# Kernel optimization log

Measured on AMD Instinct MI355X. Metric: run time of the kernel, lower is better.

## Reference

```python
import jax, jax.numpy as jnp
import numpy as np

IN_CH = 512
OUT_CH = 512
NUM_GROUPS = 32
EPS = 1e-5


def setup_inputs() -> dict:
    key = jax.random.key(0)
    ks = jax.random.split(key, 8)
    N, C, H, W = 4, IN_CH, 64, 64
    s = 0.02
    return {
        "x": jax.random.normal(ks[0], (N, C, H, W), jnp.float32),
        "gn_scale": jnp.ones((C,), jnp.float32),
        "gn_bias": jnp.zeros((C,), jnp.float32),
        "wq": jax.random.normal(ks[1], (OUT_CH, C), jnp.float32) * s,
        "bq": jnp.zeros((OUT_CH,), jnp.float32),
        "wk": jax.random.normal(ks[2], (OUT_CH, C), jnp.float32) * s,
        "bk": jnp.zeros((OUT_CH,), jnp.float32),
        "wv": jax.random.normal(ks[3], (OUT_CH, C), jnp.float32) * s,
        "bv": jnp.zeros((OUT_CH,), jnp.float32),
        "wo": jax.random.normal(ks[4], (OUT_CH, OUT_CH), jnp.float32) * s,
        "bo": jnp.zeros((OUT_CH,), jnp.float32),
    }


def _group_norm(x, scale, bias):
    # x: [N, C, H, W] -> normalize per (group, spatial)
    N, C, H, W = x.shape
    g = x.reshape(N, NUM_GROUPS, C // NUM_GROUPS, H, W)
    mean = jnp.mean(g, axis=(2, 3, 4), keepdims=True)
    var = jnp.var(g, axis=(2, 3, 4), keepdims=True)
    g = (g - mean) * jax.lax.rsqrt(var + EPS)
    h = g.reshape(N, C, H, W)
    return h * scale[None, :, None, None] + bias[None, :, None, None]


def _conv1x1(x, w, b):
    # x: [N, C_in, H, W], w: [C_out, C_in] -> [N, C_out, H, W]
    return jnp.einsum('nchw,dc->ndhw', x, w) + b[None, :, None, None]


def reference(x, gn_scale, gn_bias, wq, bq, wk, bk, wv, bv, wo, bo):
    N, C, H, W = x.shape
    L = H * W
    h = _group_norm(x, gn_scale, gn_bias)
    q = _conv1x1(h, wq, bq).reshape(N, OUT_CH, L)
    k = _conv1x1(h, wk, bk).reshape(N, OUT_CH, L)
    v = _conv1x1(h, wv, bv).reshape(N, OUT_CH, L)
    scores = jnp.einsum('nci,ncj->nij', q, k) * (OUT_CH ** -0.5)  # [N, L, L]
    att = jax.nn.softmax(scores, axis=-1)
    out = jnp.einsum('nij,ncj->nci', att, v).reshape(N, OUT_CH, H, W)
    out = _conv1x1(out, wo, bo)
    return out + x  # skip_proj is Identity since in_ch == out_ch
```

## Files before the change

### kernel.cpp

```cpp
#include <hip/hip_runtime.h>
#include <math.h>

#define NB   4
#define CCH  512
#define LL   4096
#define GRP  32
#define CPG  16
#define CL   (CCH*LL)
#define EPSV 1e-5f

typedef __bf16 bf16x8 __attribute__((ext_vector_type(8)));
typedef float  f32x4  __attribute__((ext_vector_type(4)));

#define GLOAD_LDS16(g, l) __builtin_amdgcn_global_load_lds( \
    (const __attribute__((address_space(1))) void*)(g),     \
    (__attribute__((address_space(3))) void*)(l), 16, 0, 0)

__device__ __forceinline__ int swz_slot(int row, int q) {
    return (4 * row + (q ^ (row & 3))) ^ (((row >> 2) & 1) << 2);
}
__device__ __forceinline__ void swz_src(int l, int& jj, int& cc) {
    jj = ((l >> 3) << 1) | (((l >> 2) ^ (l >> 4)) & 1);
    cc = (l & 3) ^ (jj & 3);
}

#define DPPF(x, ctrl) __builtin_bit_cast(float, \
    __builtin_amdgcn_update_dpp(0, __builtin_bit_cast(int, (x)), (ctrl), 0xf, 0xf, false))
__device__ __forceinline__ float red_max16(float x) {
    x = fmaxf(x, DPPF(x, 0xB1)); x = fmaxf(x, DPPF(x, 0x4E));
    x = fmaxf(x, DPPF(x, 0x124)); x = fmaxf(x, DPPF(x, 0x128));
    return x;
}
__device__ __forceinline__ float red_sum16(float x) {
    x += DPPF(x, 0xB1); x += DPPF(x, 0x4E);
    x += DPPF(x, 0x124); x += DPPF(x, 0x128);
    return x;
}

__global__ __launch_bounds__(1024) void gn_stats(const float* __restrict__ x,
                                                 float* __restrict__ stats) {
    int n = blockIdx.x >> 5, g = blockIdx.x & 31;
    size_t base = ((size_t)n * CCH + (size_t)g * CPG) * LL;
    const float4* xp = (const float4*)(x + base);
    const int NV = CPG * LL / 4;
    int tid = threadIdx.x;
    float s1 = 0.f, s2 = 0.f;
    for (int i = tid; i < NV; i += 1024) {
        float4 v = xp[i];
        s1 += v.x + v.y + v.z + v.w;
        s2 += v.x*v.x + v.y*v.y + v.z*v.z + v.w*v.w;
    }
    __shared__ float red[32];
    for (int o = 32; o; o >>= 1) { s1 += __shfl_down(s1, o); s2 += __shfl_down(s2, o); }
    int lane = tid & 63, w = tid >> 6;
    if (!lane) { red[w] = s1; red[16 + w] = s2; }
    __syncthreads();
    if (tid == 0) {
        float a = 0.f, b = 0.f;
        for (int i = 0; i < 16; ++i) { a += red[i]; b += red[16 + i]; }
        const float inv_n = 1.f / (float)(CPG * LL);
        float mean = a * inv_n;
        float var  = b * inv_n - mean * mean;
        stats[blockIdx.x * 2]     = mean;
        stats[blockIdx.x * 2 + 1] = rsqrtf(var + EPSV);
    }
}

__global__ __launch_bounds__(256) void gn_norm_t(const float* __restrict__ x,
    const float* __restrict__ gamma, const float* __restrict__ beta,
    const float* __restrict__ stats, __bf16* __restrict__ Ht) {
    __shared__ float T[64][65];
    int n = blockIdx.z, c0 = blockIdx.y * 64, l0 = blockIdx.x * 64;
    int tid = threadIdx.x;
    int lx = tid & 63, py = tid >> 6;
    const float* xb = x + (size_t)n * CL;
#pragma unroll
    for (int p = 0; p < 16; ++p) {
        int cl = p * 4 + py;
        int c = c0 + cl;
        int g = c >> 4;
        float mean = stats[(n * GRP + g) * 2];
        float rstd = stats[(n * GRP + g) * 2 + 1];
        float sc = gamma[c] * rstd, bi = beta[c] - mean * sc;
        float v = xb[(size_t)c * LL + l0 + lx];
        T[lx][cl] = v * sc + bi;
    }
    __syncthreads();
    __bf16* hb = Ht + (size_t)n * CL;
#pragma unroll
    for (int p = 0; p < 16; ++p) {
        int ll = p * 4 + py;
        hb[(size_t)(l0 + ll) * CCH + c0 + lx] = (__bf16)T[ll][lx];
    }
}

__global__ __launch_bounds__(256) void tobf16(const float* __restrict__ src,
                                              __bf16* __restrict__ dst, int n) {
    int i = (blockIdx.x * 256 + threadIdx.x) * 4;
    if (i < n) {
        float4 v = *(const float4*)(src + i);
        dst[i]   = (__bf16)v.x; dst[i+1] = (__bf16)v.y;
        dst[i+2] = (__bf16)v.z; dst[i+3] = (__bf16)v.w;
    }
}

#define BM 128
#define BN 128
#define BK 32

template<int EPI>
__global__ __launch_bounds__(256) void gemm_nt(
    const __bf16* __restrict__ A, const __bf16* __restrict__ B,
    void* __restrict__ Cv, int M, int N, int K,
    long bsA, long bsB, long bsC, long bsR,
    const float* __restrict__ bias, const float* __restrict__ resid, float alpha)
{
    __shared__ __align__(16) __bf16 As[BM * BK];
    __shared__ __align__(16) __bf16 Bs[BN * BK];
    const int tid = threadIdx.x;
    const int l = tid & 63, w = tid >> 6;
    const int wm = w >> 1, wn = w & 1;
    const int m0 = blockIdx.y * BM, n0 = blockIdx.x * BN;
    A += (long)blockIdx.z * bsA;
    B += (long)blockIdx.z * bsB;

    f32x4 acc[4][4];
#pragma unroll
    for (int i = 0; i < 4; ++i)
#pragma unroll
        for (int j = 0; j < 4; ++j) acc[i][j] = f32x4{0.f, 0.f, 0.f, 0.f};

    int jj, cc; swz_src(l, jj, cc);
    const int slot = swz_slot(l & 15, l >> 4);

    const __bf16* Ag = A + (size_t)(m0 + w * 16 + jj) * K + cc * 8;
    const __bf16* Bg = B + (size_t)(n0 + w * 16 + jj) * K + cc * 8;
    char* AsB = (char*)As + w * 1024;
    char* BsB = (char*)Bs + w * 1024;

    for (int k0 = 0; k0 < K; k0 += BK) {
        GLOAD_LDS16(Ag + k0,                 AsB);
        GLOAD_LDS16(Ag + k0 + (size_t)64*K,  AsB + 4096);
        GLOAD_LDS16(Bg + k0,                 BsB);
        GLOAD_LDS16(Bg + k0 + (size_t)64*K,  BsB + 4096);
        __syncthreads();
        bf16x8 ar[4], br[4];
#pragma unroll
        for (int t = 0; t < 4; ++t) {
            ar[t] = *(const bf16x8*)(As + (wm*64 + t*16) * BK + slot * 8);
            br[t] = *(const bf16x8*)(Bs + (wn*64 + t*16) * BK + slot * 8);
        }
#pragma unroll
        for (int ti = 0; ti < 4; ++ti)
#pragma unroll
            for (int tj = 0; tj < 4; ++tj)
                acc[ti][tj] = __builtin_amdgcn_mfma_f32_16x16x32_bf16(
                    ar[ti], br[tj], acc[ti][tj], 0, 0, 0);
        __syncthreads();
    }

    const long cb = (long)blockIdx.z * bsC;
#pragma unroll
    for (int ti = 0; ti < 4; ++ti) {
#pragma unroll
        for (int r = 0; r < 4; ++r) {
            int m = m0 + wm*64 + ti*16 + (l >> 4)*4 + r;
            float bv = (EPI == 2 || EPI == 4) ? bias[m] : 0.f;
#pragma unroll
            for (int tj = 0; tj < 4; ++tj) {
                int n = n0 + wn*64 + tj*16 + (l & 15);
                float v = acc[ti][tj][r];
                if (EPI == 1) v += bias[n];
                if (EPI == 2 || EPI == 4) v += bv;
                if (EPI == 4) {
                    float rs = resid[(long)blockIdx.z * bsR + (size_t)m * N + n];
                    ((float*)Cv)[cb + (size_t)m * N + n] = v + rs;
                } else {
                    ((__bf16*)Cv)[cb + (size_t)m * N + n] = (__bf16)v;
                }
            }
        }
    }
}

#define PSTR 88

__global__ __launch_bounds__(512, 2) void flash_attn(
    const __bf16* __restrict__ Qt, const __bf16* __restrict__ Kt,
    const __bf16* __restrict__ Vb, __bf16* __restrict__ Ot)
{
    __shared__ __align__(16) __bf16 Ks[16 * 64 * 32];
    __shared__ __align__(16) __bf16 Vs[2 * 512 * 32];
    __shared__ __align__(16) float  Sm[64 * 68];
    __shared__ __align__(16) __bf16 Ps[64 * PSTR];
    __shared__ float scl[64];
    __shared__ float lnv[64];

    const int tid = threadIdx.x;
    const int l = tid & 63, w = tid >> 6;
    const int wi = w & 3, kh = w >> 2;
    const int g = l >> 4, c = l & 15;
    const int b = blockIdx.x >> 6;
    const int i0 = (blockIdx.x & 63) * 64;
    const size_t bb = (size_t)b * CL;
    const float alpha = 0.044194173824159216f;

    int jj, cc; swz_src(l, jj, cc);
    const int slot = swz_slot(c, g);

    bf16x8 Qf[8];
    {
        const __bf16* Qg = Qt + bb + (size_t)(i0 + wi*16 + c) * CCH + kh*256 + g*8;
#pragma unroll
        for (int kc = 0; kc < 8; ++kc) Qf[kc] = *(const bf16x8*)(Qg + kc * 32);
    }

    f32x4 Oacc[4][4];
#pragma unroll
    for (int mi = 0; mi < 4; ++mi)
#pragma unroll
        for (int ni = 0; ni < 4; ++ni) Oacc[mi][ni] = f32x4{0.f, 0.f, 0.f, 0.f};
    float m_r[4], l_r[4];
#pragma unroll
    for (int r = 0; r < 4; ++r) { m_r[r] = -1e30f; l_r[r] = 0.f; }

    const __bf16* Kb = Kt + bb;
    const __bf16* Vg = Vb + bb;

    auto stageK = [&](int j0) {
#pragma unroll
        for (int q = 0; q < 2; ++q) {
            int kc = q * 8 + w;
#pragma unroll
            for (int p = 0; p < 4; ++p) {
                const __bf16* src = Kb + (size_t)(j0 + p*16 + jj) * CCH + kc*32 + cc*8;
                GLOAD_LDS16(src, (char*)Ks + kc*4096 + p*1024);
            }
        }
    };
    auto stageV = [&](int j0) {
#pragma unroll
        for (int jc = 0; jc < 2; ++jc)
#pragma unroll
            for (int p = 0; p < 4; ++p) {
                const __bf16* src = Vg + (size_t)(w*64 + p*16 + jj) * LL + j0 + jc*32 + cc*8;
                GLOAD_LDS16(src, (char*)Vs + jc*32768 + (w*64 + p*16)*64);
            }
    };

    stageK(0);
    for (int t = 0; t < 64; ++t) {
        __syncthreads();
        stageV(t * 64);

        f32x4 S[4];
#pragma unroll
        for (int tj = 0; tj < 4; ++tj) S[tj] = f32x4{0.f, 0.f, 0.f, 0.f};
#pragma unroll
        for (int kc = 0; kc < 8; ++kc) {
#pragma unroll
            for (int tj = 0; tj < 4; ++tj) {
                bf16x8 kf = *(const bf16x8*)(Ks + (kh*8 + kc)*2048 + tj*512 + slot*8);
                S[tj] = __builtin_amdgcn_mfma_f32_16x16x32_bf16(Qf[kc], kf, S[tj], 0, 0, 0);
            }
        }

        if (kh) {
#pragma unroll
            for (int tj = 0; tj < 4; ++tj)
#pragma unroll
                for (int r = 0; r < 4; ++r)
                    Sm[(wi*16 + g*4 + r)*68 + tj*16 + c] = S[tj][r];
        }
        __syncthreads();

        if (!kh) {
#pragma unroll
            for (int r = 0; r < 4; ++r) {
                float mt = -1e30f;
#pragma unroll
                for (int tj = 0; tj < 4; ++tj) {
                    S[tj][r] = (S[tj][r] + Sm[(wi*16 + g*4 + r)*68 + tj*16 + c]) * alpha;
                    mt = fmaxf(mt, S[tj][r]);
                }
                mt = red_max16(mt);
                float mn = fmaxf(m_r[r], mt);
                float a = __expf(m_r[r] - mn);
                m_r[r] = mn;
                int row = wi*16 + g*4 + r;
                float rs = 0.f;
#pragma unroll
                for (int tj = 0; tj < 4; ++tj) {
                    float p = __expf(S[tj][r] - mn);
                    rs += p;
                    Ps[row * PSTR + tj*16 + c] = (__bf16)p;
                }
                rs = red_sum16(rs);
                l_r[r] = l_r[r] * a + rs;
                if (c == 0) scl[row] = a;
            }
        } else {
            if (t < 63) stageK((t + 1) * 64);
        }
        __syncthreads();
        if (t < 63 && !kh) stageK((t + 1) * 64);

#pragma unroll
        for (int mi = 0; mi < 4; ++mi)
#pragma unroll
            for (int r = 0; r < 4; ++r) {
                float s = scl[mi*16 + g*4 + r];
#pragma unroll
                for (int ni = 0; ni < 4; ++ni) Oacc[mi][ni][r] *= s;
            }

#pragma unroll
        for (int jc = 0; jc < 2; ++jc) {
            bf16x8 pa[4];
#pragma unroll
            for (int mi = 0; mi < 4; ++mi)
                pa[mi] = *(const bf16x8*)(Ps + (mi*16 + c) * PSTR + jc*32 + g*8);
#pragma unroll
            for (int ni = 0; ni < 4; ++ni) {
                bf16x8 vf = *(const bf16x8*)(Vs + jc*16384 + (w*64 + ni*16)*32 + slot*8);
#pragma unroll
                for (int mi = 0; mi < 4; ++mi)
                    Oacc[mi][ni] = __builtin_amdgcn_mfma_f32_16x16x32_bf16(pa[mi], vf, Oacc[mi][ni], 0, 0, 0);
            }
        }
    }

    if (!kh && c == 0) {
#pragma unroll
        for (int r = 0; r < 4; ++r) lnv[wi*16 + g*4 + r] = 1.f / l_r[r];
    }
    __syncthreads();
#pragma unroll
    for (int mi = 0; mi < 4; ++mi) {
#pragma unroll
        for (int r = 0; r < 4; ++r) {
            int row = mi*16 + g*4 + r;
            float inv = lnv[row];
#pragma unroll
            for (int ni = 0; ni < 4; ++ni) {
                int col = w*64 + ni*16 + c;
                Ot[bb + (size_t)(i0 + row) * CCH + col] = (__bf16)(Oacc[mi][ni][r] * inv);
            }
        }
    }
}

extern "C" void kernel_launch(void* const* d_in, const int* in_sizes, int n_in,
                              void* d_out, int out_size, void* d_ws, size_t ws_size,
                              hipStream_t stream) {
    const float* x   = (const float*)d_in[0];
    const float* gnw = (const float*)d_in[1];
    const float* gnb = (const float*)d_in[2];
    const float* wq  = (const float*)d_in[3];
    const float* bq  = (const float*)d_in[4];
    const float* wk  = (const float*)d_in[5];
    const float* bk  = (const float*)d_in[6];
    const float* wv  = (const float*)d_in[7];
    const float* bv  = (const float*)d_in[8];
    const float* wo  = (const float*)d_in[9];
    const float* bo  = (const float*)d_in[10];
    float* out = (float*)d_out;

    __bf16* wsb = (__bf16*)d_ws;
    const size_t NCL = (size_t)NB * CL;
    __bf16* Ht = wsb;
    __bf16* Qt = Ht + NCL;
    __bf16* Kt = Qt + NCL;
    __bf16* Vb = Kt + NCL;
    __bf16* Ot = Vb + NCL;
    __bf16* Wb = Ot + NCL;
    float* stats = (float*)(Wb + (size_t)4 * CCH * CCH);
    __bf16* wqb = Wb;
    __bf16* wkb = Wb + (size_t)CCH * CCH;
    __bf16* wvb = Wb + (size_t)2 * CCH * CCH;
    __bf16* wob = Wb + (size_t)3 * CCH * CCH;

    tobf16<<<256, 256, 0, stream>>>(wq, wqb, CCH * CCH);
    tobf16<<<256, 256, 0, stream>>>(wk, wkb, CCH * CCH);
    tobf16<<<256, 256, 0, stream>>>(wv, wvb, CCH * CCH);
    tobf16<<<256, 256, 0, stream>>>(wo, wob, CCH * CCH);

    gn_stats<<<NB * GRP, 1024, 0, stream>>>(x, stats);
    gn_norm_t<<<dim3(LL / 64, CCH / 64, NB), 256, 0, stream>>>(x, gnw, gnb, stats, Ht);

    gemm_nt<1><<<dim3(CCH / 128, LL / 128, NB), 256, 0, stream>>>(
        Ht, wqb, Qt, LL, CCH, CCH, CL, 0, CL, 0, bq, nullptr, 1.f);
    gemm_nt<1><<<dim3(CCH / 128, LL / 128, NB), 256, 0, stream>>>(
        Ht, wkb, Kt, LL, CCH, CCH, CL, 0, CL, 0, bk, nullptr, 1.f);
    gemm_nt<2><<<dim3(LL / 128, CCH / 128, NB), 256, 0, stream>>>(
        wvb, Ht, Vb, CCH, LL, CCH, 0, CL, CL, 0, bv, nullptr, 1.f);

    flash_attn<<<dim3(NB * (LL / 64)), 512, 0, stream>>>(Qt, Kt, Vb, Ot);

    gemm_nt<4><<<dim3(LL / 128, CCH / 128, NB), 256, 0, stream>>>(
        wob, Ot, (void*)out, CCH, LL, CCH, 0, CL, CL, CL, bo, x, 1.f);
}
```

Before: 427.2 us.

## Shrink flash attention tiles to 32 queries and 32 keys with 4 waves

Restructures the flash attention kernel from 64x64 tiles with 8 waves to 32x32 tiles with 4 waves (256 threads), doubling the grid to 512 blocks with an interleaved batch/query-tile mapping. Each wave now accumulates 128 output channels, the LDS swizzle pattern is simplified, and the K prefetch is done only by the kh waves after the softmax barrier. The Oacc rescale is skipped when every row's scale factor is 1. Smaller tiles lower LDS use and may raise occupancy, but they halve reuse per loaded K/V tile and double the number of loop iterations and barriers.

```diff
diff --git a/kernel.cpp b/kernel.cpp
--- a/kernel.cpp
+++ b/kernel.cpp
@@ -17,11 +17,11 @@
     (__attribute__((address_space(3))) void*)(l), 16, 0, 0)
 
 __device__ __forceinline__ int swz_slot(int row, int q) {
-    return (4 * row + (q ^ (row & 3))) ^ (((row >> 2) & 1) << 2);
+    return 4 * row + (q ^ ((row >> 1) & 3));
 }
 __device__ __forceinline__ void swz_src(int l, int& jj, int& cc) {
-    jj = ((l >> 3) << 1) | (((l >> 2) ^ (l >> 4)) & 1);
-    cc = (l & 3) ^ (jj & 3);
+    jj = l >> 2;
+    cc = (l & 3) ^ ((l >> 3) & 3);
 }
 
 #define DPPF(x, ctrl) __builtin_bit_cast(float, \
@@ -183,25 +183,26 @@
     }
 }
 
-#define PSTR 88
-
-__global__ __launch_bounds__(512, 2) void flash_attn(
+#define PST2 40
+
+__global__ __launch_bounds__(256, 2) void flash_attn(
     const __bf16* __restrict__ Qt, const __bf16* __restrict__ Kt,
     const __bf16* __restrict__ Vb, __bf16* __restrict__ Ot)
 {
-    __shared__ __align__(16) __bf16 Ks[16 * 64 * 32];
-    __shared__ __align__(16) __bf16 Vs[2 * 512 * 32];
-    __shared__ __align__(16) float  Sm[64 * 68];
-    __shared__ __align__(16) __bf16 Ps[64 * PSTR];
-    __shared__ float scl[64];
-    __shared__ float lnv[64];
+    __shared__ __align__(16) __bf16 Ks[16 * 1024];
+    __shared__ __align__(16) __bf16 Vs[512 * 32];
+    __shared__ float  Sm[32 * 33];
+    __shared__ __align__(16) __bf16 Ps[32 * PST2];
+    __shared__ float scl[32];
+    __shared__ float lnv[32];
 
     const int tid = threadIdx.x;
     const int l = tid & 63, w = tid >> 6;
-    const int wi = w & 3, kh = w >> 2;
+    const int wi = w & 1, kh = w >> 1;
     const int g = l >> 4, c = l & 15;
-    const int b = blockIdx.x >> 6;
-    const int i0 = (blockIdx.x & 63) * 64;
+    const int b = (blockIdx.x & 7) >> 1;
+    const int qt = ((blockIdx.x >> 3) << 1) | (blockIdx.x & 1);
+    const int i0 = qt * 32;
     const size_t bb = (size_t)b * CL;
     const float alpha = 0.044194173824159216f;
 
@@ -215,11 +216,11 @@
         for (int kc = 0; kc < 8; ++kc) Qf[kc] = *(const bf16x8*)(Qg + kc * 32);
     }
 
-    f32x4 Oacc[4][4];
-#pragma unroll
-    for (int mi = 0; mi < 4; ++mi)
-#pragma unroll
-        for (int ni = 0; ni < 4; ++ni) Oacc[mi][ni] = f32x4{0.f, 0.f, 0.f, 0.f};
+    f32x4 Oacc[2][8];
+#pragma unroll
+    for (int mi = 0; mi < 2; ++mi)
+#pragma unroll
+        for (int ni = 0; ni < 8; ++ni) Oacc[mi][ni] = f32x4{0.f, 0.f, 0.f, 0.f};
     float m_r[4], l_r[4];
 #pragma unroll
     for (int r = 0; r < 4; ++r) { m_r[r] = -1e30f; l_r[r] = 0.f; }
@@ -227,106 +228,118 @@
     const __bf16* Kb = Kt + bb;
     const __bf16* Vg = Vb + bb;
 
-    auto stageK = [&](int j0) {
-#pragma unroll
-        for (int q = 0; q < 2; ++q) {
-            int kc = q * 8 + w;
-#pragma unroll
-            for (int p = 0; p < 4; ++p) {
-                const __bf16* src = Kb + (size_t)(j0 + p*16 + jj) * CCH + kc*32 + cc*8;
-                GLOAD_LDS16(src, (char*)Ks + kc*4096 + p*1024);
-            }
-        }
-    };
-    auto stageV = [&](int j0) {
-#pragma unroll
-        for (int jc = 0; jc < 2; ++jc)
-#pragma unroll
-            for (int p = 0; p < 4; ++p) {
-                const __bf16* src = Vg + (size_t)(w*64 + p*16 + jj) * LL + j0 + jc*32 + cc*8;
-                GLOAD_LDS16(src, (char*)Vs + jc*32768 + (w*64 + p*16)*64);
-            }
-    };
-
-    stageK(0);
-    for (int t = 0; t < 64; ++t) {
+    {
+        const int j0 = 0;
+#pragma unroll
+        for (int q = 0; q < 4; ++q) {
+            int kc = q * 4 + w;
+#pragma unroll
+            for (int sub = 0; sub < 2; ++sub) {
+                const __bf16* src = Kb + (size_t)(j0 + sub*16 + jj) * CCH + kc*32 + cc*8;
+                GLOAD_LDS16(src, (char*)Ks + kc*2048 + sub*1024);
+            }
+        }
+    }
+
+    for (int t = 0; t < 128; ++t) {
         __syncthreads();
-        stageV(t * 64);
-
-        f32x4 S[4];
-#pragma unroll
-        for (int tj = 0; tj < 4; ++tj) S[tj] = f32x4{0.f, 0.f, 0.f, 0.f};
+        {
+            const int j0 = t * 32;
+#pragma unroll
+            for (int p = 0; p < 8; ++p) {
+                const __bf16* src = Vg + (size_t)(w*128 + p*16 + jj) * LL + j0 + cc*8;
+                GLOAD_LDS16(src, (char*)Vs + (w*128 + p*16) * 64);
+            }
+        }
+
+        f32x4 S[2];
+        S[0] = f32x4{0.f,0.f,0.f,0.f}; S[1] = f32x4{0.f,0.f,0.f,0.f};
 #pragma unroll
         for (int kc = 0; kc < 8; ++kc) {
 #pragma unroll
-            for (int tj = 0; tj < 4; ++tj) {
-                bf16x8 kf = *(const bf16x8*)(Ks + (kh*8 + kc)*2048 + tj*512 + slot*8);
+            for (int tj = 0; tj < 2; ++tj) {
+                bf16x8 kf = *(const bf16x8*)(Ks + (kh*8 + kc)*1024 + tj*512 + slot*8);
                 S[tj] = __builtin_amdgcn_mfma_f32_16x16x32_bf16(Qf[kc], kf, S[tj], 0, 0, 0);
             }
         }
-
         if (kh) {
 #pragma unroll
-            for (int tj = 0; tj < 4; ++tj)
+            for (int tj = 0; tj < 2; ++tj)
 #pragma unroll
                 for (int r = 0; r < 4; ++r)
-                    Sm[(wi*16 + g*4 + r)*68 + tj*16 + c] = S[tj][r];
+                    Sm[(wi*16 + g*4 + r)*33 + tj*16 + c] = S[tj][r];
         }
         __syncthreads();
 
         if (!kh) {
 #pragma unroll
             for (int r = 0; r < 4; ++r) {
+                int row = wi*16 + g*4 + r;
                 float mt = -1e30f;
 #pragma unroll
-                for (int tj = 0; tj < 4; ++tj) {
-                    S[tj][r] = (S[tj][r] + Sm[(wi*16 + g*4 + r)*68 + tj*16 + c]) * alpha;
+                for (int tj = 0; tj < 2; ++tj) {
+                    S[tj][r] = (S[tj][r] + Sm[row*33 + tj*16 + c]) * alpha;
                     mt = fmaxf(mt, S[tj][r]);
                 }
                 mt = red_max16(mt);
                 float mn = fmaxf(m_r[r], mt);
                 float a = __expf(m_r[r] - mn);
                 m_r[r] = mn;
-                int row = wi*16 + g*4 + r;
                 float rs = 0.f;
 #pragma unroll
-                for (int tj = 0; tj < 4; ++tj) {
+                for (int tj = 0; tj < 2; ++tj) {
                     float p = __expf(S[tj][r] - mn);
                     rs += p;
-                    Ps[row * PSTR + tj*16 + c] = (__bf16)p;
+                    Ps[row * PST2 + tj*16 + c] = (__bf16)p;
                 }
                 rs = red_sum16(rs);
                 l_r[r] = l_r[r] * a + rs;
                 if (c == 0) scl[row] = a;
             }
-        } else {
-            if (t < 63) stageK((t + 1) * 64);
         }
         __syncthreads();
-        if (t < 63 && !kh) stageK((t + 1) * 64);
-
-#pragma unroll
-        for (int mi = 0; mi < 4; ++mi)
+
+        if (kh && t < 127) {
+            const int j0 = (t + 1) * 32;
+#pragma unroll
+            for (int q = 0; q < 8; ++q) {
+                int kc = q * 2 + (w & 1);
+#pragma unroll
+                for (int sub = 0; sub < 2; ++sub) {
+                    const __bf16* src = Kb + (size_t)(j0 + sub*16 + jj) * CCH + kc*32 + cc*8;
+                    GLOAD_LDS16(src, (char*)Ks + kc*2048 + sub*1024);
+                }
+            }
+        }
+
+        float sv[2][4];
+        bool need = false;
+#pragma unroll
+        for (int mi = 0; mi < 2; ++mi)
 #pragma unroll
             for (int r = 0; r < 4; ++r) {
-                float s = scl[mi*16 + g*4 + r];
-#pragma unroll
-                for (int ni = 0; ni < 4; ++ni) Oacc[mi][ni][r] *= s;
-            }
-
-#pragma unroll
-        for (int jc = 0; jc < 2; ++jc) {
-            bf16x8 pa[4];
-#pragma unroll
-            for (int mi = 0; mi < 4; ++mi)
-                pa[mi] = *(const bf16x8*)(Ps + (mi*16 + c) * PSTR + jc*32 + g*8);
-#pragma unroll
-            for (int ni = 0; ni < 4; ++ni) {
-                bf16x8 vf = *(const bf16x8*)(Vs + jc*16384 + (w*64 + ni*16)*32 + slot*8);
-#pragma unroll
-                for (int mi = 0; mi < 4; ++mi)
-                    Oacc[mi][ni] = __builtin_amdgcn_mfma_f32_16x16x32_bf16(pa[mi], vf, Oacc[mi][ni], 0, 0, 0);
-            }
+                sv[mi][r] = scl[mi*16 + g*4 + r];
+                need = need || (sv[mi][r] != 1.0f);
+            }
+        if (__any(need)) {
+#pragma unroll
+            for (int mi = 0; mi < 2; ++mi)
+#pragma unroll
+                for (int r = 0; r < 4; ++r)
+#pragma unroll
+                    for (int ni = 0; ni < 8; ++ni) Oacc[mi][ni][r] *= sv[mi][r];
+        }
+
+        bf16x8 pa[2];
+#pragma unroll
+        for (int mi = 0; mi < 2; ++mi)
+            pa[mi] = *(const bf16x8*)(Ps + (mi*16 + c) * PST2 + g*8);
+#pragma unroll
+        for (int ni = 0; ni < 8; ++ni) {
+            bf16x8 vf = *(const bf16x8*)(Vs + (w*128 + ni*16)*32 + slot*8);
+#pragma unroll
+            for (int mi = 0; mi < 2; ++mi)
+                Oacc[mi][ni] = __builtin_amdgcn_mfma_f32_16x16x32_bf16(pa[mi], vf, Oacc[mi][ni], 0, 0, 0);
         }
     }
 
@@ -336,14 +349,14 @@
     }
     __syncthreads();
 #pragma unroll
-    for (int mi = 0; mi < 4; ++mi) {
+    for (int mi = 0; mi < 2; ++mi) {
 #pragma unroll
         for (int r = 0; r < 4; ++r) {
             int row = mi*16 + g*4 + r;
             float inv = lnv[row];
 #pragma unroll
-            for (int ni = 0; ni < 4; ++ni) {
-                int col = w*64 + ni*16 + c;
+            for (int ni = 0; ni < 8; ++ni) {
+                int col = w*128 + ni*16 + c;
                 Ot[bb + (size_t)(i0 + row) * CCH + col] = (__bf16)(Oacc[mi][ni][r] * inv);
             }
         }
@@ -395,7 +408,7 @@
     gemm_nt<2><<<dim3(LL / 128, CCH / 128, NB), 256, 0, stream>>>(
         wvb, Ht, Vb, CCH, LL, CCH, 0, CL, CL, 0, bv, nullptr, 1.f);
 
-    flash_attn<<<dim3(NB * (LL / 64)), 512, 0, stream>>>(Qt, Kt, Vb, Ot);
+    flash_attn<<<dim3(512), 256, 0, stream>>>(Qt, Kt, Vb, Ot);
 
     gemm_nt<4><<<dim3(LL / 128, CCH / 128, NB), 256, 0, stream>>>(
         wob, Ot, (void*)out, CCH, LL, CCH, 0, CL, CL, CL, bo, x, 1.f);
```

After: 510.6 us. +19.5%, slower.
